# Kernel optimization log

Measured on AMD Instinct MI355X. Metric: run time of the kernel, lower is better.

Reference implementation:

```python
import jax, jax.numpy as jnp
import numpy as np

B, H, M, D, MID, DV = 128, 8, 196, 128, 64, 128


def setup_inputs() -> dict:
    key0 = jax.random.key(0)
    ks = jax.random.split(key0, 12)
    query = jax.random.normal(ks[0], (B, H, D), dtype=jnp.float32)
    key = jax.random.normal(ks[1], (B, H, M, D), dtype=jnp.float32)
    att_mask = jax.random.randint(ks[2], (B, M), 0, 2).astype(jnp.float32)
    att_mask = att_mask.at[:, 0].set(1.0)  # guarantee each row has >=1 valid slot
    value1 = jax.random.normal(ks[3], (B, H, DV), dtype=jnp.float32)
    value2 = jax.random.normal(ks[4], (B, H, M, DV), dtype=jnp.float32)
    W_basic = jax.random.normal(ks[5], (D, MID), dtype=jnp.float32) * 0.05
    b_basic = jnp.zeros((MID,), dtype=jnp.float32)
    W_spatial = jax.random.normal(ks[6], (MID, 1), dtype=jnp.float32) * 0.05
    b_spatial = jnp.zeros((1,), dtype=jnp.float32)
    W_channel = jax.random.normal(ks[7], (MID, DV), dtype=jnp.float32) * 0.05
    b_channel = jnp.zeros((DV,), dtype=jnp.float32)
    return {
        'query': query, 'key': key, 'att_mask': att_mask,
        'value1': value1, 'value2': value2,
        'W_basic': W_basic, 'b_basic': b_basic,
        'W_spatial': W_spatial, 'b_spatial': b_spatial,
        'W_channel': W_channel, 'b_channel': b_channel,
    }


def reference(query, key, att_mask, value1, value2,
              W_basic, b_basic, W_spatial, b_spatial, W_channel, b_channel):
    # att_map: broadcast elementwise QK product  [B,H,M,D]
    att_map = query[..., None, :] * key
    # attention_basic: Linear + ReLU (Dropout is identity at eval)  [B,H,M,MID]
    h = jax.nn.relu(jnp.einsum('bhmd,de->bhme', att_map, W_basic) + b_basic)
    # masked mean-pool over regions  [B,H,MID]
    mask_ext = att_mask[:, None, :, None]  # [B,1,M,1]
    att_map_pool = jnp.sum(h * mask_ext, axis=-2) / jnp.sum(mask_ext, axis=-2)
    # spatial attention logits  [B,H,M]
    alpha_spatial = (jnp.einsum('bhme,eo->bhmo', h, W_spatial) + b_spatial)[..., 0]
    alpha_spatial = jnp.where(att_mask[:, None, :] == 0, -1e9, alpha_spatial)
    alpha_spatial = jax.nn.softmax(alpha_spatial, axis=-1)
    # weighted sum over regions  [B,H,DV]
    v2 = jnp.einsum('bhm,bhmv->bhv', alpha_spatial, value2)
    # channel gate  [B,H,DV]
    alpha_channel = jax.nn.sigmoid(jnp.einsum('bhe,ev->bhv', att_map_pool, W_channel) + b_channel)
    return value1 * v2 * alpha_channel
```

## Files before the change

kernel.cpp:

```cpp
#include <hip/hip_runtime.h>
#include <cstddef>

#define NBH  1024
#define Mm   196
#define Dd   128
#define MIDe 64
#define DVv  128
#define WQLD 136

typedef __attribute__((ext_vector_type(8))) short bf16x8;
typedef __attribute__((ext_vector_type(4))) float f32x4;

__device__ __forceinline__ short f2bf(float x) {
    union { float f; unsigned u; } v; v.f = x;
    return (short)((v.u + 0x7FFFu + ((v.u >> 16) & 1u)) >> 16);
}

__device__ __forceinline__ float waveReduceSum(float v) {
#pragma unroll
    for (int off = 32; off > 0; off >>= 1) v += __shfl_xor(v, off, 64);
    return v;
}

__device__ __forceinline__ float waveReduceMax(float v) {
#pragma unroll
    for (int off = 32; off > 0; off >>= 1) v = fmaxf(v, __shfl_xor(v, off, 64));
    return v;
}

__global__ __launch_bounds__(256, 4)
void scatt_fused(const float* __restrict__ query,
                 const float* __restrict__ key,
                 const float* __restrict__ att_mask,
                 const float* __restrict__ value1,
                 const float* __restrict__ value2,
                 const float* __restrict__ W_basic,
                 const float* __restrict__ b_basic,
                 const float* __restrict__ W_spatial,
                 const float* __restrict__ b_spatial,
                 const float* __restrict__ W_channel,
                 const float* __restrict__ b_channel,
                 float* __restrict__ out)
{
    __shared__ short wqT[MIDe][WQLD];
    __shared__ float qS[Dd];
    __shared__ float maskS[Mm];
    __shared__ float sS[Mm];
    __shared__ float poolPart[4][MIDe];
    __shared__ float poolS[MIDe];
    __shared__ float partS[8][DVv];
    __shared__ float redS[12];

    const int t    = threadIdx.x;
    const int lane = t & 63;
    const int w    = t >> 6;
    const int ln15 = lane & 15;
    const int q4   = lane >> 4;
    const int bh   = blockIdx.x;
    const int b    = bh >> 3;

    const float* __restrict__ keyB  = key      + (size_t)bh * Mm * Dd;
    const float* __restrict__ val2B = value2   + (size_t)bh * Mm * DVv;
    const float* __restrict__ qB    = query    + (size_t)bh * Dd;
    const float* __restrict__ maskB = att_mask + (size_t)b  * Mm;

    if (t < 32) ((float4*)qS)[t] = ((const float4*)qB)[t];
    for (int i = t; i < Mm; i += 256) maskS[i] = maskB[i];
    __syncthreads();

    {
        const int e0 = lane;
        const int d0 = w * 32;
#pragma unroll
        for (int c = 0; c < 4; ++c) {
            short pk[8];
#pragma unroll
            for (int j = 0; j < 8; ++j) {
                const int d = d0 + c * 8 + j;
                pk[j] = f2bf(qS[d] * W_basic[d * MIDe + e0]);
            }
            *(bf16x8*)&wqT[e0][d0 + c * 8] = *(bf16x8*)pk;
        }
    }
    __syncthreads();

    bf16x8 bfr[4][4];
#pragma unroll
    for (int ks = 0; ks < 4; ++ks)
#pragma unroll
        for (int nt = 0; nt < 4; ++nt)
            bfr[ks][nt] = *(const bf16x8*)&wqT[nt * 16 + ln15][ks * 32 + q4 * 8];

    float bbv[4], wspv[4];
#pragma unroll
    for (int nt = 0; nt < 4; ++nt) {
        bbv[nt]  = b_basic[nt * 16 + ln15];
        wspv[nt] = W_spatial[nt * 16 + ln15];
    }
    const float bsp = b_spatial[0];
    float poolAcc[4] = {0.f, 0.f, 0.f, 0.f};

    for (int mt = w; mt < 13; mt += 4) {
        const int mrow = min(mt * 16 + ln15, Mm - 1);
        const float* ap = keyB + (size_t)mrow * Dd + q4 * 8;
        float4 a0[4], a1[4];
#pragma unroll
        for (int ks = 0; ks < 4; ++ks) {
            a0[ks] = *(const float4*)(ap + ks * 32);
            a1[ks] = *(const float4*)(ap + ks * 32 + 4);
        }
        f32x4 acc[4] = {f32x4{0,0,0,0}, f32x4{0,0,0,0},
                        f32x4{0,0,0,0}, f32x4{0,0,0,0}};
#pragma unroll
        for (int ks = 0; ks < 4; ++ks) {
            const bf16x8 af = { f2bf(a0[ks].x), f2bf(a0[ks].y),
                                f2bf(a0[ks].z), f2bf(a0[ks].w),
                                f2bf(a1[ks].x), f2bf(a1[ks].y),
                                f2bf(a1[ks].z), f2bf(a1[ks].w) };
#pragma unroll
            for (int nt = 0; nt < 4; ++nt)
                acc[nt] = __builtin_amdgcn_mfma_f32_16x16x32_bf16(
                              af, bfr[ks][nt], acc[nt], 0, 0, 0);
        }
#pragma unroll
        for (int r = 0; r < 4; ++r) {
            const int m = mt * 16 + q4 * 4 + r;
            const bool valid = m < Mm;
            const float msk = valid ? maskS[m] : 0.f;
            float srow = 0.f;
#pragma unroll
            for (int nt = 0; nt < 4; ++nt) {
                float hv = acc[nt][r] + bbv[nt];
                hv = hv > 0.f ? hv : 0.f;
                poolAcc[nt] = fmaf(hv, msk, poolAcc[nt]);
                srow = fmaf(hv, wspv[nt], srow);
            }
            srow += __shfl_xor(srow, 1, 64);
            srow += __shfl_xor(srow, 2, 64);
            srow += __shfl_xor(srow, 4, 64);
            srow += __shfl_xor(srow, 8, 64);
            if (valid && ln15 == 0) sS[m] = srow + bsp;
        }
    }
#pragma unroll
    for (int nt = 0; nt < 4; ++nt) {
        poolAcc[nt] += __shfl_xor(poolAcc[nt], 16, 64);
        poolAcc[nt] += __shfl_xor(poolAcc[nt], 32, 64);
    }
    if (lane < 16) {
#pragma unroll
        for (int nt = 0; nt < 4; ++nt)
            poolPart[w][nt * 16 + lane] = poolAcc[nt];
    }
    __syncthreads();

    const float myMask = (t < Mm) ? maskS[t] : 0.f;
    float myS = -3.0e38f;
    if (t < Mm) {
        myS = sS[t];
        if (myMask == 0.f) myS = -1.0e9f;
    }
    const float rmx = waveReduceMax(myS);
    if (lane == 0) redS[w] = rmx;
    __syncthreads();
    const float mx = fmaxf(fmaxf(redS[0], redS[1]), fmaxf(redS[2], redS[3]));
    const float ev = (t < Mm) ? __expf(myS - mx) : 0.f;
    const float s1 = waveReduceSum(ev);
    const float s2 = waveReduceSum(myMask);
    if (lane == 0) { redS[4 + w] = s1; redS[8 + w] = s2; }
    __syncthreads();
    const float denom = redS[4] + redS[5] + redS[6] + redS[7];
    const float cnt   = redS[8] + redS[9] + redS[10] + redS[11];
    if (t < Mm) sS[t] = ev / denom;
    if (t < MIDe)
        poolS[t] = (poolPart[0][t] + poolPart[1][t] + poolPart[2][t] + poolPart[3][t]) / cnt;
    __syncthreads();

    float chv = 0.f;
    if (t < DVv) {
        float a = b_channel[t];
#pragma unroll 8
        for (int e = 0; e < MIDe; ++e)
            a = fmaf(poolS[e], W_channel[e * DVv + t], a);
        chv = 1.f / (1.f + __expf(-a));
    }

    const int vq = t & 31;
    const int ms = t >> 5;
    float4 acc4 = make_float4(0.f, 0.f, 0.f, 0.f);
#pragma unroll 5
    for (int m = ms; m < Mm; m += 8) {
        const float a = sS[m];
        const float4 vv = *(const float4*)(val2B + (size_t)m * DVv + 4 * vq);
        acc4.x = fmaf(a, vv.x, acc4.x);
        acc4.y = fmaf(a, vv.y, acc4.y);
        acc4.z = fmaf(a, vv.z, acc4.z);
        acc4.w = fmaf(a, vv.w, acc4.w);
    }
    ((float4*)&partS[ms][0])[vq] = acc4;
    __syncthreads();

    if (t < DVv) {
        float v2v = 0.f;
#pragma unroll
        for (int i = 0; i < 8; ++i) v2v += partS[i][t];
        out[(size_t)bh * DVv + t] = value1[(size_t)bh * DVv + t] * v2v * chv;
    }
}

extern "C" void kernel_launch(void* const* d_in, const int* in_sizes, int n_in,
                              void* d_out, int out_size, void* d_ws, size_t ws_size,
                              hipStream_t stream) {
    const float* query     = (const float*)d_in[0];
    const float* key       = (const float*)d_in[1];
    const float* att_mask  = (const float*)d_in[2];
    const float* value1    = (const float*)d_in[3];
    const float* value2    = (const float*)d_in[4];
    const float* W_basic   = (const float*)d_in[5];
    const float* b_basic   = (const float*)d_in[6];
    const float* W_spatial = (const float*)d_in[7];
    const float* b_spatial = (const float*)d_in[8];
    const float* W_channel = (const float*)d_in[9];
    const float* b_channel = (const float*)d_in[10];
    float* out = (float*)d_out;

    scatt_fused<<<NBH, 256, 0, stream>>>(query, key, att_mask, value1, value2,
                                         W_basic, b_basic, W_spatial, b_spatial,
                                         W_channel, b_channel, out);
}
```

Measured before the change: 243.2 us.

## Fuse online softmax and value2 weighted sum into the MFMA tile loop

Each wave now issues its value2 row loads alongside the key loads for the same 16-row tile. It keeps a running max, sum and weighted value accumulator (online softmax), then merges the per-wave partials at the end. This removes the separate softmax pass, the later value2 sweep and several block barriers, and lets the value2 fetch overlap the MFMA work. The B fragments are now re-read from LDS inside the loop instead of being held in registers, which lowers register pressure but adds LDS traffic and extra exp work per lane.

```diff
diff --git a/kernel.cpp b/kernel.cpp
--- a/kernel.cpp
+++ b/kernel.cpp
@@ -19,12 +19,6 @@
 __device__ __forceinline__ float waveReduceSum(float v) {
 #pragma unroll
     for (int off = 32; off > 0; off >>= 1) v += __shfl_xor(v, off, 64);
-    return v;
-}
-
-__device__ __forceinline__ float waveReduceMax(float v) {
-#pragma unroll
-    for (int off = 32; off > 0; off >>= 1) v = fmaxf(v, __shfl_xor(v, off, 64));
     return v;
 }
 
@@ -45,11 +39,10 @@
     __shared__ short wqT[MIDe][WQLD];
     __shared__ float qS[Dd];
     __shared__ float maskS[Mm];
-    __shared__ float sS[Mm];
     __shared__ float poolPart[4][MIDe];
     __shared__ float poolS[MIDe];
-    __shared__ float partS[8][DVv];
-    __shared__ float redS[12];
+    __shared__ float accW[4][DVv];
+    __shared__ float mW[4], lW[4], cntW[4];
 
     const int t    = threadIdx.x;
     const int lane = t & 63;
@@ -84,13 +77,6 @@
     }
     __syncthreads();
 
-    bf16x8 bfr[4][4];
-#pragma unroll
-    for (int ks = 0; ks < 4; ++ks)
-#pragma unroll
-        for (int nt = 0; nt < 4; ++nt)
-            bfr[ks][nt] = *(const bf16x8*)&wqT[nt * 16 + ln15][ks * 32 + q4 * 8];
-
     float bbv[4], wspv[4];
 #pragma unroll
     for (int nt = 0; nt < 4; ++nt) {
@@ -98,7 +84,11 @@
         wspv[nt] = W_spatial[nt * 16 + ln15];
     }
     const float bsp = b_spatial[0];
+
     float poolAcc[4] = {0.f, 0.f, 0.f, 0.f};
+    float m_run = -3.0e38f;
+    float l_run = 0.f;
+    float2 av   = make_float2(0.f, 0.f);
 
     for (int mt = w; mt < 13; mt += 4) {
         const int mrow = min(mt * 16 + ln15, Mm - 1);
@@ -109,6 +99,16 @@
             a0[ks] = *(const float4*)(ap + ks * 32);
             a1[ks] = *(const float4*)(ap + ks * 32 + 4);
         }
+        float2 vv[16];
+        {
+            const float* vp = val2B + 2 * lane;
+#pragma unroll
+            for (int i = 0; i < 16; ++i) {
+                const int mc = min(mt * 16 + i, Mm - 1);
+                vv[i] = *(const float2*)(vp + (size_t)mc * DVv);
+            }
+        }
+
         f32x4 acc[4] = {f32x4{0,0,0,0}, f32x4{0,0,0,0},
                         f32x4{0,0,0,0}, f32x4{0,0,0,0}};
 #pragma unroll
@@ -118,10 +118,15 @@
                                 f2bf(a1[ks].x), f2bf(a1[ks].y),
                                 f2bf(a1[ks].z), f2bf(a1[ks].w) };
 #pragma unroll
-            for (int nt = 0; nt < 4; ++nt)
+            for (int nt = 0; nt < 4; ++nt) {
+                const bf16x8 bk =
+                    *(const bf16x8*)&wqT[nt * 16 + ln15][ks * 32 + q4 * 8];
                 acc[nt] = __builtin_amdgcn_mfma_f32_16x16x32_bf16(
-                              af, bfr[ks][nt], acc[nt], 0, 0, 0);
-        }
+                              af, bk, acc[nt], 0, 0, 0);
+            }
+        }
+
+        float sR[4];
 #pragma unroll
         for (int r = 0; r < 4; ++r) {
             const int m = mt * 16 + q4 * 4 + r;
@@ -139,9 +144,32 @@
             srow += __shfl_xor(srow, 2, 64);
             srow += __shfl_xor(srow, 4, 64);
             srow += __shfl_xor(srow, 8, 64);
-            if (valid && ln15 == 0) sS[m] = srow + bsp;
-        }
-    }
+            sR[r] = valid ? (msk == 0.f ? -1.0e9f : srow + bsp) : -3.0e38f;
+        }
+
+        float sv[16];
+#pragma unroll
+        for (int i = 0; i < 16; ++i)
+            sv[i] = __shfl(sR[i & 3], (i >> 2) << 4, 64);
+
+        float tm = sv[0];
+#pragma unroll
+        for (int i = 1; i < 16; ++i) tm = fmaxf(tm, sv[i]);
+
+        const float newm = fmaxf(m_run, tm);
+        const float sc = __expf(m_run - newm);
+        m_run = newm;
+        l_run *= sc;
+        av.x *= sc; av.y *= sc;
+#pragma unroll
+        for (int i = 0; i < 16; ++i) {
+            const float p = __expf(sv[i] - newm);
+            l_run += p;
+            av.x = fmaf(p, vv[i].x, av.x);
+            av.y = fmaf(p, vv[i].y, av.y);
+        }
+    }
+
 #pragma unroll
     for (int nt = 0; nt < 4; ++nt) {
         poolAcc[nt] += __shfl_xor(poolAcc[nt], 16, 64);
@@ -152,58 +180,41 @@
         for (int nt = 0; nt < 4; ++nt)
             poolPart[w][nt * 16 + lane] = poolAcc[nt];
     }
-    __syncthreads();
-
-    const float myMask = (t < Mm) ? maskS[t] : 0.f;
-    float myS = -3.0e38f;
-    if (t < Mm) {
-        myS = sS[t];
-        if (myMask == 0.f) myS = -1.0e9f;
-    }
-    const float rmx = waveReduceMax(myS);
-    if (lane == 0) redS[w] = rmx;
-    __syncthreads();
-    const float mx = fmaxf(fmaxf(redS[0], redS[1]), fmaxf(redS[2], redS[3]));
-    const float ev = (t < Mm) ? __expf(myS - mx) : 0.f;
-    const float s1 = waveReduceSum(ev);
-    const float s2 = waveReduceSum(myMask);
-    if (lane == 0) { redS[4 + w] = s1; redS[8 + w] = s2; }
-    __syncthreads();
-    const float denom = redS[4] + redS[5] + redS[6] + redS[7];
-    const float cnt   = redS[8] + redS[9] + redS[10] + redS[11];
-    if (t < Mm) sS[t] = ev / denom;
-    if (t < MIDe)
-        poolS[t] = (poolPart[0][t] + poolPart[1][t] + poolPart[2][t] + poolPart[3][t]) / cnt;
-    __syncthreads();
-
-    float chv = 0.f;
+    {
+        const int mi = w * 64 + lane;
+        float cm = (mi < Mm) ? maskS[mi] : 0.f;
+        cm = waveReduceSum(cm);
+        if (lane == 0) cntW[w] = cm;
+    }
+    if (lane == 0) { mW[w] = m_run; lW[w] = l_run; }
+    ((float2*)&accW[w][0])[lane] = av;
+    __syncthreads();
+
+    float v2v = 0.f;
+    if (t < DVv) {
+        const float M = fmaxf(fmaxf(mW[0], mW[1]), fmaxf(mW[2], mW[3]));
+        float L = 0.f;
+#pragma unroll
+        for (int i = 0; i < 4; ++i) {
+            const float s = __expf(mW[i] - M);
+            L   = fmaf(lW[i], s, L);
+            v2v = fmaf(accW[i][t], s, v2v);
+        }
+        v2v /= L;
+    }
+    if (t < MIDe) {
+        const float cnt = cntW[0] + cntW[1] + cntW[2] + cntW[3];
+        poolS[t] = (poolPart[0][t] + poolPart[1][t] +
+                    poolPart[2][t] + poolPart[3][t]) / cnt;
+    }
+    __syncthreads();
+
     if (t < DVv) {
         float a = b_channel[t];
 #pragma unroll 8
         for (int e = 0; e < MIDe; ++e)
             a = fmaf(poolS[e], W_channel[e * DVv + t], a);
-        chv = 1.f / (1.f + __expf(-a));
-    }
-
-    const int vq = t & 31;
-    const int ms = t >> 5;
-    float4 acc4 = make_float4(0.f, 0.f, 0.f, 0.f);
-#pragma unroll 5
-    for (int m = ms; m < Mm; m += 8) {
-        const float a = sS[m];
-        const float4 vv = *(const float4*)(val2B + (size_t)m * DVv + 4 * vq);
-        acc4.x = fmaf(a, vv.x, acc4.x);
-        acc4.y = fmaf(a, vv.y, acc4.y);
-        acc4.z = fmaf(a, vv.z, acc4.z);
-        acc4.w = fmaf(a, vv.w, acc4.w);
-    }
-    ((float4*)&partS[ms][0])[vq] = acc4;
-    __syncthreads();
-
-    if (t < DVv) {
-        float v2v = 0.f;
-#pragma unroll
-        for (int i = 0; i < 8; ++i) v2v += partS[i][t];
+        const float chv = 1.f / (1.f + __expf(-a));
         out[(size_t)bh * DVv + t] = value1[(size_t)bh * DVv + t] * v2v * chv;
     }
 }
```

Result: slower. 268.1 us (+10.3%).
